# Performance work log

Measured on AMD Instinct MI355X. Metric: run time of the kernel, lower is better.

Reference implementation:

```python
import jax, jax.numpy as jnp
import numpy as np

B, N, K = 64, 1024, 16  # graphs per batch, nodes per graph, top-k (k=16 hardcoded in module)
EPS = 1e-20


def setup_inputs() -> dict:
    key = jax.random.key(0)
    ks = jax.random.split(key, 6)
    C = 128
    x = jax.random.normal(ks[0], (B * N, C), jnp.float32)
    pos = jax.random.normal(ks[1], (B * N, 3), jnp.float32)
    W1 = jax.random.normal(ks[2], (C, C), jnp.float32) / np.sqrt(C).astype(np.float32)
    b1 = jnp.zeros((C,), jnp.float32)
    gamma = jnp.ones((C,), jnp.float32)
    beta = jnp.zeros((C,), jnp.float32)
    W2 = jax.random.normal(ks[3], (C, 10), jnp.float32) / np.sqrt(C).astype(np.float32)
    b2 = jnp.zeros((10,), jnp.float32)
    t = jnp.ones((1,), jnp.float32)
    return dict(x=x, pos=pos, W1=W1, b1=b1, gamma=gamma, beta=beta, W2=W2, b2=b2, t=t)


def _edge_arrays(idx):
    # idx: (B, N, K) per-target top-k source node indices (graph-local)
    offs = (jnp.arange(B, dtype=jnp.int32) * N)[:, None, None]
    src = (idx + offs).reshape(-1)
    tgt = (jnp.broadcast_to(jnp.arange(N, dtype=jnp.int32)[None, :, None], (B, N, K)) + offs).reshape(-1)
    return jnp.stack([src, tgt])  # (2, B*N*K)


def _knn_edges(pos):
    # KNNGraph(k=16) on positions, loop=False (exclude self)
    p = pos.reshape(B, N, 3)
    d2 = jnp.sum((p[:, :, None, :] - p[:, None, :, :]) ** 2, axis=-1)  # (B,N,N)
    d2 = d2 + jnp.eye(N, dtype=d2.dtype) * 1e10
    _, idx = jax.lax.top_k(-d2, K)  # nearest K per node
    return _edge_arrays(idx)


def reference(x, pos, W1, b1, gamma, beta, W2, b2, t):
    key = jax.random.key(42)
    k1, k2 = jax.random.split(key)
    # tg MLP: lin -> batchnorm -> relu -> lin (training-mode batch stats over nodes)
    h = x @ W1 + b1
    mu = h.mean(axis=0)
    var = h.var(axis=0)
    h = (h - mu) / jnp.sqrt(var + 1e-5) * gamma + beta
    h = jax.nn.relu(h)
    emb = h @ W2 + b2  # (B*N, 10)
    emb = emb + jax.random.uniform(k1, emb.shape, emb.dtype) * 0.001
    e = emb.reshape(B, N, 10)
    # pairwise distances per graph (vectorized over the python loop in the original)
    diff = e[:, :, None, :] - e[:, None, :, :]  # (B,N,N,10)
    dist = jnp.linalg.norm(diff, axis=-1)  # (B,N,N)
    p = jnp.exp(-t[0] * dist ** 2)
    u = jax.random.uniform(k2, p.shape, p.dtype)
    gumbel = -jnp.log(-jnp.log(u + EPS) + EPS)
    noisy_logits = jnp.log(p + EPS) + gumbel
    # torch topk over dim=0 (sources) for each target column -> transpose then top_k on last axis
    vals, idx = jax.lax.top_k(jnp.swapaxes(noisy_logits, 1, 2), K)  # (B,N,K)
    vals = jax.nn.softmax(vals, axis=-1)
    vals = vals / vals.max(axis=-1, keepdims=True)
    soft_idx = _edge_arrays(idx)  # (2, B*N*K)
    knn_idx = _knn_edges(pos)
    edge_index = jnp.concatenate([soft_idx, knn_idx], axis=1)
    return vals.reshape(-1), soft_idx, edge_index
```

## Files before the change

kernel.cpp:

```cpp
#include <hip/hip_runtime.h>
#include <stdint.h>
#include <math.h>

#define BG 64
#define NG 1024
#define KK 16
#define CC 128
#define NNODE (BG * NG)
#define NSOFT (BG * NG * KK)
#define FEPS 1e-20f

__host__ __device__ __forceinline__ uint32_t rotl32u(uint32_t x, int r) {
  return (x << r) | (x >> (32 - r));
}

__host__ __device__ __forceinline__ void tf2x32(uint32_t k0, uint32_t k1,
                                                uint32_t x0, uint32_t x1,
                                                uint32_t &o0, uint32_t &o1) {
  uint32_t k2 = k0 ^ k1 ^ 0x1BD11BDAu;
  x0 += k0; x1 += k1;
#define TFR(r) { x0 += x1; x1 = rotl32u(x1, r); x1 ^= x0; }
  TFR(13) TFR(15) TFR(26) TFR(6)
  x0 += k1; x1 += k2 + 1u;
  TFR(17) TFR(29) TFR(16) TFR(24)
  x0 += k2; x1 += k0 + 2u;
  TFR(13) TFR(15) TFR(26) TFR(6)
  x0 += k0; x1 += k1 + 3u;
  TFR(17) TFR(29) TFR(16) TFR(24)
  x0 += k1; x1 += k2 + 4u;
  TFR(13) TFR(15) TFR(26) TFR(6)
  x0 += k2; x1 += k0 + 5u;
#undef TFR
  o0 = x0; o1 = x1;
}

__device__ __forceinline__ float jax_uniform01(uint32_t ka, uint32_t kb, uint32_t m) {
  uint32_t o0, o1;
  tf2x32(ka, kb, 0u, m, o0, o1);
  uint32_t bits = o0 ^ o1;
  float f = __uint_as_float((bits >> 9) | 0x3f800000u) - 1.0f;
  return fmaxf(f, 0.0f);
}

__device__ __forceinline__ int vbin_soft(float v) {
  float fb = (v + 50.0f) * (256.0f / 67.0f);
  fb = fminf(fmaxf(fb, 0.0f), 255.0f);
  return (int)fb;
}
__device__ __forceinline__ int vbin_knn(float v) {
  float fb = (v + 64.0f) * 4.0f;
  fb = fminf(fmaxf(fb, 0.0f), 255.0f);
  return (int)fb;
}

#define LDS_WAIT() asm volatile("s_waitcnt lgkmcnt(0)" ::: "memory")

__global__ __launch_bounds__(256) void k_gemm1(const float* __restrict__ x,
                                               const float* __restrict__ W1,
                                               const float* __restrict__ b1,
                                               float* __restrict__ h) {
  __shared__ __align__(16) float xs[64 * 128];
  const int t = threadIdx.x;
  const size_t blockBase = (size_t)blockIdx.x * (64 * 128);
  #pragma unroll
  for (int j = 0; j < 32; ++j) xs[t + j * 256] = x[blockBase + t + j * 256];
  __syncthreads();
  const int c = t & 127;
  const int rg = t >> 7;
  float acc[32];
  #pragma unroll
  for (int j = 0; j < 32; ++j) acc[j] = 0.f;
  const float* xrow = &xs[rg * 32 * 128];
  for (int k4 = 0; k4 < 128; k4 += 4) {
    const float w0 = W1[(size_t)(k4 + 0) * 128 + c];
    const float w1 = W1[(size_t)(k4 + 1) * 128 + c];
    const float w2 = W1[(size_t)(k4 + 2) * 128 + c];
    const float w3 = W1[(size_t)(k4 + 3) * 128 + c];
    #pragma unroll
    for (int j = 0; j < 32; ++j) {
      const float4 xv = *(const float4*)&xrow[j * 128 + k4];
      acc[j] = fmaf(xv.x, w0, acc[j]);
      acc[j] = fmaf(xv.y, w1, acc[j]);
      acc[j] = fmaf(xv.z, w2, acc[j]);
      acc[j] = fmaf(xv.w, w3, acc[j]);
    }
  }
  const float bb = b1[c];
  #pragma unroll
  for (int j = 0; j < 32; ++j)
    h[blockBase + (size_t)(rg * 32 + j) * 128 + c] = acc[j] + bb;
}

__global__ __launch_bounds__(256) void k_bn_part(const float* __restrict__ h,
                                                 float* __restrict__ p1,
                                                 float* __restrict__ p2) {
  const int t = threadIdx.x;
  const int cg = t & 31;
  const int rg = t >> 5;
  const size_t rowBase = (size_t)blockIdx.x * 256;
  float s1[4] = {0, 0, 0, 0}, s2[4] = {0, 0, 0, 0};
  for (int i = 0; i < 32; ++i) {
    const size_t r = rowBase + (size_t)i * 8 + rg;
    const float4 v = *(const float4*)&h[r * 128 + cg * 4];
    s1[0] += v.x; s2[0] = fmaf(v.x, v.x, s2[0]);
    s1[1] += v.y; s2[1] = fmaf(v.y, v.y, s2[1]);
    s1[2] += v.z; s2[2] = fmaf(v.z, v.z, s2[2]);
    s1[3] += v.w; s2[3] = fmaf(v.w, v.w, s2[3]);
  }
  __shared__ float red1[8 * 128];
  __shared__ float red2[8 * 128];
  #pragma unroll
  for (int i = 0; i < 4; ++i) {
    red1[rg * 128 + cg * 4 + i] = s1[i];
    red2[rg * 128 + cg * 4 + i] = s2[i];
  }
  __syncthreads();
  if (t < 128) {
    float a = 0.f;
    #pragma unroll
    for (int g = 0; g < 8; ++g) a += red1[g * 128 + t];
    p1[(size_t)blockIdx.x * 128 + t] = a;
  } else {
    const int c = t - 128;
    float a = 0.f;
    #pragma unroll
    for (int g = 0; g < 8; ++g) a += red2[g * 128 + c];
    p2[(size_t)blockIdx.x * 128 + c] = a;
  }
}

__global__ __launch_bounds__(128) void k_bn_final(const float* __restrict__ p1,
                                                  const float* __restrict__ p2,
                                                  const float* __restrict__ gamma,
                                                  const float* __restrict__ beta,
                                                  float* __restrict__ scale,
                                                  float* __restrict__ shift) {
  const int c = threadIdx.x;
  float s1 = 0.f, s2 = 0.f;
  for (int b = 0; b < 256; ++b) {
    s1 += p1[b * 128 + c];
    s2 += p2[b * 128 + c];
  }
  const float mu = s1 * (1.0f / NNODE);
  float var = s2 * (1.0f / NNODE) - mu * mu;
  var = fmaxf(var, 0.f);
  const float sc = gamma[c] / sqrtf(var + 1e-5f);
  scale[c] = sc;
  shift[c] = beta[c] - mu * sc;
}

__global__ __launch_bounds__(256) void k_emb(const float* __restrict__ h,
                                             const float* __restrict__ scale,
                                             const float* __restrict__ shift,
                                             const float* __restrict__ W2,
                                             const float* __restrict__ b2,
                                             float* __restrict__ e,
                                             uint32_t ka, uint32_t kb) {
  __shared__ __align__(16) float hn[64 * 132];
  const int t = threadIdx.x;
  const int rowBase = blockIdx.x * 64;
  {
    const int c = t & 127;
    const float sc = scale[c], sh = shift[c];
    #pragma unroll
    for (int j = 0; j < 32; ++j) {
      const int r = (t >> 7) + j * 2;
      const float v = fmaf(h[(size_t)(rowBase + r) * 128 + c], sc, sh);
      hn[r * 132 + c] = fmaxf(v, 0.f);
    }
  }
  __syncthreads();
  #pragma unroll
  for (int j = 0; j < 3; ++j) {
    const int o = t + j * 256;
    if (o < 640) {
      const int r = o / 10;
      const int col = o - r * 10;
      float acc = 0.f;
      for (int k4 = 0; k4 < 128; k4 += 4) {
        const float4 hv = *(const float4*)&hn[r * 132 + k4];
        acc = fmaf(hv.x, W2[(k4 + 0) * 10 + col], acc);
        acc = fmaf(hv.y, W2[(k4 + 1) * 10 + col], acc);
        acc = fmaf(hv.z, W2[(k4 + 2) * 10 + col], acc);
        acc = fmaf(hv.w, W2[(k4 + 3) * 10 + col], acc);
      }
      acc += b2[col];
      const uint32_t m = (uint32_t)(rowBase + r) * 10u + (uint32_t)col;
      const float u = jax_uniform01(ka, kb, m);
      e[(size_t)(rowBase + r) * 10 + col] = acc + u * 0.001f;
    }
  }
}

__global__ __launch_bounds__(512) void k_soft(const float* __restrict__ e,
                                              const float* __restrict__ tsc,
                                              float* __restrict__ out,
                                              uint32_t ka, uint32_t kb) {
  __shared__ uint32_t bins[8][256];
  __shared__ float    cv[8][64];
  __shared__ int      cidx[8][64];
  __shared__ uint32_t cnt[8];
  __shared__ float    o16v[8][16];
  __shared__ int      o16i[8][16];

  const int t = threadIdx.x, lane = t & 63, w = t >> 6;
  const int node = blockIdx.x * 8 + w;
  const int b = node >> 10, jt = node & (NG - 1);
  const float negt = -tsc[0];
  const float* eg = e + (size_t)b * (NG * 10);

  { uint4 z = {0, 0, 0, 0}; *(uint4*)&bins[w][lane * 4] = z; }
  if (lane == 0) cnt[w] = 0u;
  LDS_WAIT();

  float ej[10];
  #pragma unroll
  for (int d = 0; d < 10; ++d) ej[d] = eg[(size_t)jt * 10 + d];

  float vv[16];
  const uint32_t mB = ((uint32_t)b << 20) + (uint32_t)jt;
  #pragma unroll
  for (int st = 0; st < 16; ++st) {
    const int s = st * 64 + lane;
    const float2* rp = (const float2*)(eg + (size_t)s * 10);
    const float2 a0 = rp[0], a1 = rp[1], a2 = rp[2], a3 = rp[3], a4 = rp[4];
    float dd, acc;
    dd = ej[0] - a0.x; acc = dd * dd;
    dd = ej[1] - a0.y; acc = fmaf(dd, dd, acc);
    dd = ej[2] - a1.x; acc = fmaf(dd, dd, acc);
    dd = ej[3] - a1.y; acc = fmaf(dd, dd, acc);
    dd = ej[4] - a2.x; acc = fmaf(dd, dd, acc);
    dd = ej[5] - a2.y; acc = fmaf(dd, dd, acc);
    dd = ej[6] - a3.x; acc = fmaf(dd, dd, acc);
    dd = ej[7] - a3.y; acc = fmaf(dd, dd, acc);
    dd = ej[8] - a4.x; acc = fmaf(dd, dd, acc);
    dd = ej[9] - a4.y; acc = fmaf(dd, dd, acc);
    const float dist = sqrtf(acc);
    const float d2 = dist * dist;
    const float p = __expf(negt * d2);
    const float u = jax_uniform01(ka, kb, mB + ((uint32_t)s << 10));
    const float li = __logf(u + FEPS);
    const float g = -__logf(FEPS - li);
    const float v = __logf(p + FEPS) + g;
    vv[st] = v;
    atomicAdd(&bins[w][vbin_soft(v)], 1u);
  }
  LDS_WAIT();

  const uint4 c4 = *(const uint4*)&bins[w][lane * 4];
  const uint32_t lsum = c4.x + c4.y + c4.z + c4.w;
  uint32_t xs = lsum;
  #pragma unroll
  for (int off = 1; off < 64; off <<= 1) {
    uint32_t tt = (uint32_t)__shfl_down((int)xs, off, 64);
    if (lane + off < 64) xs += tt;
  }
  const uint32_t after = xs - lsum;
  const uint32_t s3 = c4.w + after;
  const uint32_t s2 = c4.z + s3;
  const uint32_t s1 = c4.y + s2;
  const uint32_t s0 = c4.x + s1;
  int localB = -1;
  if (s3 >= 16u) localB = lane * 4 + 3;
  else if (s2 >= 16u) localB = lane * 4 + 2;
  else if (s1 >= 16u) localB = lane * 4 + 1;
  else if (s0 >= 16u) localB = lane * 4 + 0;
  const unsigned long long msk = __ballot(localB >= 0);
  const int hl = 63 - __builtin_clzll(msk);
  const int B = __shfl(localB, hl, 64);

  #pragma unroll
  for (int st = 0; st < 16; ++st) {
    if (vbin_soft(vv[st]) >= B) {
      const uint32_t pos = atomicAdd(&cnt[w], 1u);
      if (pos < 64u) { cv[w][pos] = vv[st]; cidx[w][pos] = st * 64 + lane; }
    }
  }
  LDS_WAIT();

  int C = (int)cnt[w]; if (C > 64) C = 64;
  const float mvv = (lane < C) ? cv[w][lane] : 0.f;
  const int   mii = (lane < C) ? cidx[w][lane] : 0;
  int rank = 0;
  for (int j = 0; j < C; ++j) {
    const float vj = cv[w][j];
    const int ij = cidx[w][j];
    if (vj > mvv || (vj == mvv && ij < mii)) ++rank;
  }
  if (lane < C && rank < 16) { o16v[w][rank] = mvv; o16i[w][rank] = mii; }
  LDS_WAIT();

  if (lane < 16) {
    const float vq = o16v[w][lane];
    const float m0 = o16v[w][0];
    float uex = __expf(vq - m0);
    float ss = uex;
    #pragma unroll
    for (int off = 1; off < 16; off <<= 1) ss += __shfl_xor(ss, off, 16);
    const float u0 = __shfl(uex, 0, 16);
    const float s0v = u0 / ss;
    const float sv = uex / ss;
    const float o = sv / s0v;
    const size_t base = (size_t)node * KK + lane;
    const float tgtf = (float)node;
    const float srcf = (float)(b * NG + o16i[w][lane]);
    out[base] = o;
    out[(size_t)NSOFT + base] = srcf;
    out[2 * (size_t)NSOFT + base] = tgtf;
    out[3 * (size_t)NSOFT + base] = srcf;
    out[5 * (size_t)NSOFT + base] = tgtf;
  }
}

__global__ __launch_bounds__(512) void k_knn(const float* __restrict__ pos,
                                             float* __restrict__ out) {
  __shared__ uint32_t bins[8][256];
  __shared__ float    cv[8][64];
  __shared__ int      cidx[8][64];
  __shared__ uint32_t cnt[8];
  __shared__ int      o16i[8][16];

  const int t = threadIdx.x, lane = t & 63, w = t >> 6;
  const int node = blockIdx.x * 8 + w;
  const int b = node >> 10, it = node & (NG - 1);
  const float* pg = pos + (size_t)b * (NG * 3);

  { uint4 z = {0, 0, 0, 0}; *(uint4*)&bins[w][lane * 4] = z; }
  if (lane == 0) cnt[w] = 0u;
  LDS_WAIT();

  const float px = pg[(size_t)it * 3 + 0];
  const float py = pg[(size_t)it * 3 + 1];
  const float pz = pg[(size_t)it * 3 + 2];

  float vv[16];
  #pragma unroll
  for (int st = 0; st < 16; ++st) {
    const int s = st * 64 + lane;
    const float qx = pg[(size_t)s * 3 + 0];
    const float qy = pg[(size_t)s * 3 + 1];
    const float qz = pg[(size_t)s * 3 + 2];
    const float dx = px - qx, dy = py - qy, dz = pz - qz;
    float d2 = dx * dx;
    d2 = fmaf(dy, dy, d2);
    d2 = fmaf(dz, dz, d2);
    if (s == it) d2 += 1e10f;
    const float v = -d2;
    vv[st] = v;
    atomicAdd(&bins[w][vbin_knn(v)], 1u);
  }
  LDS_WAIT();

  const uint4 c4 = *(const uint4*)&bins[w][lane * 4];
  const uint32_t lsum = c4.x + c4.y + c4.z + c4.w;
  uint32_t xs = lsum;
  #pragma unroll
  for (int off = 1; off < 64; off <<= 1) {
    uint32_t tt = (uint32_t)__shfl_down((int)xs, off, 64);
    if (lane + off < 64) xs += tt;
  }
  const uint32_t after = xs - lsum;
  const uint32_t s3 = c4.w + after;
  const uint32_t s2 = c4.z + s3;
  const uint32_t s1 = c4.y + s2;
  const uint32_t s0 = c4.x + s1;
  int localB = -1;
  if (s3 >= 16u) localB = lane * 4 + 3;
  else if (s2 >= 16u) localB = lane * 4 + 2;
  else if (s1 >= 16u) localB = lane * 4 + 1;
  else if (s0 >= 16u) localB = lane * 4 + 0;
  const unsigned long long msk = __ballot(localB >= 0);
  const int hl = 63 - __builtin_clzll(msk);
  const int B = __shfl(localB, hl, 64);

  #pragma unroll
  for (int st = 0; st < 16; ++st) {
    if (vbin_knn(vv[st]) >= B) {
      const uint32_t pos = atomicAdd(&cnt[w], 1u);
      if (pos < 64u) { cv[w][pos] = vv[st]; cidx[w][pos] = st * 64 + lane; }
    }
  }
  LDS_WAIT();

  int C = (int)cnt[w]; if (C > 64) C = 64;
  const float mvv = (lane < C) ? cv[w][lane] : 0.f;
  const int   mii = (lane < C) ? cidx[w][lane] : 0;
  int rank = 0;
  for (int j = 0; j < C; ++j) {
    const float vj = cv[w][j];
    const int ij = cidx[w][j];
    if (vj > mvv || (vj == mvv && ij < mii)) ++rank;
  }
  if (lane < C && rank < 16) o16i[w][rank] = mii;
  LDS_WAIT();

  if (lane < 16) {
    const size_t base = (size_t)node * KK + lane;
    out[4 * (size_t)NSOFT + base] = (float)(b * NG + o16i[w][lane]);
    out[6 * (size_t)NSOFT + base] = (float)node;
  }
}

extern "C" void kernel_launch(void* const* d_in, const int* in_sizes, int n_in,
                              void* d_out, int out_size, void* d_ws, size_t ws_size,
                              hipStream_t stream) {
  const float* x     = (const float*)d_in[0];
  const float* pos   = (const float*)d_in[1];
  const float* W1    = (const float*)d_in[2];
  const float* b1    = (const float*)d_in[3];
  const float* gamma = (const float*)d_in[4];
  const float* beta  = (const float*)d_in[5];
  const float* W2    = (const float*)d_in[6];
  const float* b2    = (const float*)d_in[7];
  const float* t     = (const float*)d_in[8];
  float* out = (float*)d_out;

  float* ws    = (float*)d_ws;
  float* h     = ws;
  float* e     = h + (size_t)NNODE * CC;
  float* p1    = e + (size_t)NNODE * 10;
  float* p2    = p1 + 256 * 128;
  float* scale = p2 + 256 * 128;
  float* shift = scale + CC;

  uint32_t k1a, k1b, k2a, k2b;
  tf2x32(0u, 42u, 0u, 0u, k1a, k1b);
  tf2x32(0u, 42u, 0u, 1u, k2a, k2b);

  k_gemm1<<<dim3(NNODE / 64), dim3(256), 0, stream>>>(x, W1, b1, h);
  k_bn_part<<<dim3(256), dim3(256), 0, stream>>>(h, p1, p2);
  k_bn_final<<<dim3(1), dim3(128), 0, stream>>>(p1, p2, gamma, beta, scale, shift);
  k_emb<<<dim3(NNODE / 64), dim3(256), 0, stream>>>(h, scale, shift, W2, b2, e, k1a, k1b);
  k_knn<<<dim3(NNODE / 8), dim3(512), 0, stream>>>(pos, out);
  k_soft<<<dim3(NNODE / 8), dim3(512), 0, stream>>>(e, t, out, k2a, k2b);
}
```

Measured before the change: 447.7 us.

## Fuse BN partial stats into GEMM, parallelize BN final, stage graph data in LDS

Measured after the change: 419.8 us. -6.2%, faster.

```diff
diff --git a/kernel.cpp b/kernel.cpp
--- a/kernel.cpp
+++ b/kernel.cpp
@@ -58,7 +58,9 @@
 __global__ __launch_bounds__(256) void k_gemm1(const float* __restrict__ x,
                                                const float* __restrict__ W1,
                                                const float* __restrict__ b1,
-                                               float* __restrict__ h) {
+                                               float* __restrict__ h,
+                                               float* __restrict__ p1,
+                                               float* __restrict__ p2) {
   __shared__ __align__(16) float xs[64 * 128];
   const int t = threadIdx.x;
   const size_t blockBase = (size_t)blockIdx.x * (64 * 128);
@@ -86,67 +88,54 @@
     }
   }
   const float bb = b1[c];
-  #pragma unroll
-  for (int j = 0; j < 32; ++j)
-    h[blockBase + (size_t)(rg * 32 + j) * 128 + c] = acc[j] + bb;
-}
-
-__global__ __launch_bounds__(256) void k_bn_part(const float* __restrict__ h,
-                                                 float* __restrict__ p1,
-                                                 float* __restrict__ p2) {
-  const int t = threadIdx.x;
-  const int cg = t & 31;
-  const int rg = t >> 5;
-  const size_t rowBase = (size_t)blockIdx.x * 256;
-  float s1[4] = {0, 0, 0, 0}, s2[4] = {0, 0, 0, 0};
-  for (int i = 0; i < 32; ++i) {
-    const size_t r = rowBase + (size_t)i * 8 + rg;
-    const float4 v = *(const float4*)&h[r * 128 + cg * 4];
-    s1[0] += v.x; s2[0] = fmaf(v.x, v.x, s2[0]);
-    s1[1] += v.y; s2[1] = fmaf(v.y, v.y, s2[1]);
-    s1[2] += v.z; s2[2] = fmaf(v.z, v.z, s2[2]);
-    s1[3] += v.w; s2[3] = fmaf(v.w, v.w, s2[3]);
-  }
-  __shared__ float red1[8 * 128];
-  __shared__ float red2[8 * 128];
-  #pragma unroll
-  for (int i = 0; i < 4; ++i) {
-    red1[rg * 128 + cg * 4 + i] = s1[i];
-    red2[rg * 128 + cg * 4 + i] = s2[i];
-  }
+  float s1 = 0.f, s2 = 0.f;
+  #pragma unroll
+  for (int j = 0; j < 32; ++j) {
+    const float v = acc[j] + bb;
+    h[blockBase + (size_t)(rg * 32 + j) * 128 + c] = v;
+    s1 += v;
+    s2 = fmaf(v, v, s2);
+  }
+  __syncthreads();
+  float* r1 = xs;
+  float* r2 = xs + 256;
+  r1[rg * 128 + c] = s1;
+  r2[rg * 128 + c] = s2;
   __syncthreads();
   if (t < 128) {
-    float a = 0.f;
-    #pragma unroll
-    for (int g = 0; g < 8; ++g) a += red1[g * 128 + t];
-    p1[(size_t)blockIdx.x * 128 + t] = a;
+    p1[(size_t)t * 1024 + blockIdx.x] = r1[t] + r1[128 + t];
   } else {
-    const int c = t - 128;
-    float a = 0.f;
-    #pragma unroll
-    for (int g = 0; g < 8; ++g) a += red2[g * 128 + c];
-    p2[(size_t)blockIdx.x * 128 + c] = a;
-  }
-}
-
-__global__ __launch_bounds__(128) void k_bn_final(const float* __restrict__ p1,
+    const int cc = t - 128;
+    p2[(size_t)cc * 1024 + blockIdx.x] = r2[cc] + r2[128 + cc];
+  }
+}
+
+__global__ __launch_bounds__(256) void k_bn_final(const float* __restrict__ p1,
                                                   const float* __restrict__ p2,
                                                   const float* __restrict__ gamma,
                                                   const float* __restrict__ beta,
                                                   float* __restrict__ scale,
                                                   float* __restrict__ shift) {
-  const int c = threadIdx.x;
-  float s1 = 0.f, s2 = 0.f;
-  for (int b = 0; b < 256; ++b) {
-    s1 += p1[b * 128 + c];
-    s2 += p2[b * 128 + c];
-  }
-  const float mu = s1 * (1.0f / NNODE);
-  float var = s2 * (1.0f / NNODE) - mu * mu;
-  var = fmaxf(var, 0.f);
-  const float sc = gamma[c] / sqrtf(var + 1e-5f);
-  scale[c] = sc;
-  shift[c] = beta[c] - mu * sc;
+  const int c = blockIdx.x, t = threadIdx.x;
+  const float* q1 = p1 + (size_t)c * 1024;
+  const float* q2 = p2 + (size_t)c * 1024;
+  float a1 = q1[t] + q1[t + 256] + q1[t + 512] + q1[t + 768];
+  float a2 = q2[t] + q2[t + 256] + q2[t + 512] + q2[t + 768];
+  __shared__ float r1[256], r2[256];
+  r1[t] = a1; r2[t] = a2;
+  __syncthreads();
+  for (int o = 128; o > 0; o >>= 1) {
+    if (t < o) { r1[t] += r1[t + o]; r2[t] += r2[t + o]; }
+    __syncthreads();
+  }
+  if (t == 0) {
+    const float mu = r1[0] * (1.0f / NNODE);
+    float var = r2[0] * (1.0f / NNODE) - mu * mu;
+    var = fmaxf(var, 0.f);
+    const float sc = gamma[c] / sqrtf(var + 1e-5f);
+    scale[c] = sc;
+    shift[c] = beta[c] - mu * sc;
+  }
 }
 
 __global__ __launch_bounds__(256) void k_emb(const float* __restrict__ h,
@@ -196,49 +185,59 @@
                                               const float* __restrict__ tsc,
                                               float* __restrict__ out,
                                               uint32_t ka, uint32_t kb) {
+  __shared__ float    els[10 * NG];
   __shared__ uint32_t bins[8][256];
-  __shared__ float    cv[8][64];
-  __shared__ int      cidx[8][64];
+  __shared__ float    cv[8][48];
+  __shared__ int      cidx[8][48];
   __shared__ uint32_t cnt[8];
   __shared__ float    o16v[8][16];
   __shared__ int      o16i[8][16];
 
   const int t = threadIdx.x, lane = t & 63, w = t >> 6;
   const int node = blockIdx.x * 8 + w;
-  const int b = node >> 10, jt = node & (NG - 1);
+  const int b = blockIdx.x >> 7;
+  const int jt = node & (NG - 1);
   const float negt = -tsc[0];
   const float* eg = e + (size_t)b * (NG * 10);
 
   { uint4 z = {0, 0, 0, 0}; *(uint4*)&bins[w][lane * 4] = z; }
   if (lane == 0) cnt[w] = 0u;
-  LDS_WAIT();
+
+  for (int s = t; s < NG; s += 512) {
+    const float2* rp = (const float2*)(eg + (size_t)s * 10);
+    const float2 a0 = rp[0], a1 = rp[1], a2 = rp[2], a3 = rp[3], a4 = rp[4];
+    els[0 * NG + s] = a0.x; els[1 * NG + s] = a0.y;
+    els[2 * NG + s] = a1.x; els[3 * NG + s] = a1.y;
+    els[4 * NG + s] = a2.x; els[5 * NG + s] = a2.y;
+    els[6 * NG + s] = a3.x; els[7 * NG + s] = a3.y;
+    els[8 * NG + s] = a4.x; els[9 * NG + s] = a4.y;
+  }
+  __syncthreads();
 
   float ej[10];
   #pragma unroll
-  for (int d = 0; d < 10; ++d) ej[d] = eg[(size_t)jt * 10 + d];
+  for (int d = 0; d < 10; ++d) ej[d] = els[d * NG + jt];
 
   float vv[16];
-  const uint32_t mB = ((uint32_t)b << 20) + (uint32_t)jt;
+  const uint32_t mL = ((uint32_t)b << 20) + (uint32_t)jt + ((uint32_t)lane << 10);
   #pragma unroll
   for (int st = 0; st < 16; ++st) {
     const int s = st * 64 + lane;
-    const float2* rp = (const float2*)(eg + (size_t)s * 10);
-    const float2 a0 = rp[0], a1 = rp[1], a2 = rp[2], a3 = rp[3], a4 = rp[4];
     float dd, acc;
-    dd = ej[0] - a0.x; acc = dd * dd;
-    dd = ej[1] - a0.y; acc = fmaf(dd, dd, acc);
-    dd = ej[2] - a1.x; acc = fmaf(dd, dd, acc);
-    dd = ej[3] - a1.y; acc = fmaf(dd, dd, acc);
-    dd = ej[4] - a2.x; acc = fmaf(dd, dd, acc);
-    dd = ej[5] - a2.y; acc = fmaf(dd, dd, acc);
-    dd = ej[6] - a3.x; acc = fmaf(dd, dd, acc);
-    dd = ej[7] - a3.y; acc = fmaf(dd, dd, acc);
-    dd = ej[8] - a4.x; acc = fmaf(dd, dd, acc);
-    dd = ej[9] - a4.y; acc = fmaf(dd, dd, acc);
+    dd = ej[0] - els[0 * NG + s]; acc = dd * dd;
+    dd = ej[1] - els[1 * NG + s]; acc = fmaf(dd, dd, acc);
+    dd = ej[2] - els[2 * NG + s]; acc = fmaf(dd, dd, acc);
+    dd = ej[3] - els[3 * NG + s]; acc = fmaf(dd, dd, acc);
+    dd = ej[4] - els[4 * NG + s]; acc = fmaf(dd, dd, acc);
+    dd = ej[5] - els[5 * NG + s]; acc = fmaf(dd, dd, acc);
+    dd = ej[6] - els[6 * NG + s]; acc = fmaf(dd, dd, acc);
+    dd = ej[7] - els[7 * NG + s]; acc = fmaf(dd, dd, acc);
+    dd = ej[8] - els[8 * NG + s]; acc = fmaf(dd, dd, acc);
+    dd = ej[9] - els[9 * NG + s]; acc = fmaf(dd, dd, acc);
     const float dist = sqrtf(acc);
     const float d2 = dist * dist;
     const float p = __expf(negt * d2);
-    const float u = jax_uniform01(ka, kb, mB + ((uint32_t)s << 10));
+    const float u = jax_uniform01(ka, kb, mL + ((uint32_t)st << 16));
     const float li = __logf(u + FEPS);
     const float g = -__logf(FEPS - li);
     const float v = __logf(p + FEPS) + g;
@@ -273,12 +272,12 @@
   for (int st = 0; st < 16; ++st) {
     if (vbin_soft(vv[st]) >= B) {
       const uint32_t pos = atomicAdd(&cnt[w], 1u);
-      if (pos < 64u) { cv[w][pos] = vv[st]; cidx[w][pos] = st * 64 + lane; }
+      if (pos < 48u) { cv[w][pos] = vv[st]; cidx[w][pos] = st * 64 + lane; }
     }
   }
   LDS_WAIT();
 
-  int C = (int)cnt[w]; if (C > 64) C = 64;
+  int C = (int)cnt[w]; if (C > 48) C = 48;
   const float mvv = (lane < C) ? cv[w][lane] : 0.f;
   const int   mii = (lane < C) ? cidx[w][lane] : 0;
   int rank = 0;
@@ -314,33 +313,40 @@
 
 __global__ __launch_bounds__(512) void k_knn(const float* __restrict__ pos,
                                              float* __restrict__ out) {
+  __shared__ float    pls[3 * NG];
   __shared__ uint32_t bins[8][256];
-  __shared__ float    cv[8][64];
-  __shared__ int      cidx[8][64];
+  __shared__ float    cv[8][48];
+  __shared__ int      cidx[8][48];
   __shared__ uint32_t cnt[8];
   __shared__ int      o16i[8][16];
 
   const int t = threadIdx.x, lane = t & 63, w = t >> 6;
   const int node = blockIdx.x * 8 + w;
-  const int b = node >> 10, it = node & (NG - 1);
+  const int b = blockIdx.x >> 7;
+  const int it = node & (NG - 1);
   const float* pg = pos + (size_t)b * (NG * 3);
 
   { uint4 z = {0, 0, 0, 0}; *(uint4*)&bins[w][lane * 4] = z; }
   if (lane == 0) cnt[w] = 0u;
-  LDS_WAIT();
-
-  const float px = pg[(size_t)it * 3 + 0];
-  const float py = pg[(size_t)it * 3 + 1];
-  const float pz = pg[(size_t)it * 3 + 2];
+
+  for (int s = t; s < NG; s += 512) {
+    pls[0 * NG + s] = pg[(size_t)s * 3 + 0];
+    pls[1 * NG + s] = pg[(size_t)s * 3 + 1];
+    pls[2 * NG + s] = pg[(size_t)s * 3 + 2];
+  }
+  __syncthreads();
+
+  const float px = pls[0 * NG + it];
+  const float py = pls[1 * NG + it];
+  const float pz = pls[2 * NG + it];
 
   float vv[16];
   #pragma unroll
   for (int st = 0; st < 16; ++st) {
     const int s = st * 64 + lane;
-    const float qx = pg[(size_t)s * 3 + 0];
-    const float qy = pg[(size_t)s * 3 + 1];
-    const float qz = pg[(size_t)s * 3 + 2];
-    const float dx = px - qx, dy = py - qy, dz = pz - qz;
+    const float dx = px - pls[0 * NG + s];
+    const float dy = py - pls[1 * NG + s];
+    const float dz = pz - pls[2 * NG + s];
     float d2 = dx * dx;
     d2 = fmaf(dy, dy, d2);
     d2 = fmaf(dz, dz, d2);
@@ -377,12 +383,12 @@
   for (int st = 0; st < 16; ++st) {
     if (vbin_knn(vv[st]) >= B) {
       const uint32_t pos = atomicAdd(&cnt[w], 1u);
-      if (pos < 64u) { cv[w][pos] = vv[st]; cidx[w][pos] = st * 64 + lane; }
+      if (pos < 48u) { cv[w][pos] = vv[st]; cidx[w][pos] = st * 64 + lane; }
     }
   }
   LDS_WAIT();
 
-  int C = (int)cnt[w]; if (C > 64) C = 64;
+  int C = (int)cnt[w]; if (C > 48) C = 48;
   const float mvv = (lane < C) ? cv[w][lane] : 0.f;
   const int   mii = (lane < C) ? cidx[w][lane] : 0;
   int rank = 0;
@@ -419,17 +425,16 @@
   float* h     = ws;
   float* e     = h + (size_t)NNODE * CC;
   float* p1    = e + (size_t)NNODE * 10;
-  float* p2    = p1 + 256 * 128;
-  float* scale = p2 + 256 * 128;
+  float* p2    = p1 + 128 * 1024;
+  float* scale = p2 + 128 * 1024;
   float* shift = scale + CC;
 
   uint32_t k1a, k1b, k2a, k2b;
   tf2x32(0u, 42u, 0u, 0u, k1a, k1b);
   tf2x32(0u, 42u, 0u, 1u, k2a, k2b);
 
-  k_gemm1<<<dim3(NNODE / 64), dim3(256), 0, stream>>>(x, W1, b1, h);
-  k_bn_part<<<dim3(256), dim3(256), 0, stream>>>(h, p1, p2);
-  k_bn_final<<<dim3(1), dim3(128), 0, stream>>>(p1, p2, gamma, beta, scale, shift);
+  k_gemm1<<<dim3(NNODE / 64), dim3(256), 0, stream>>>(x, W1, b1, h, p1, p2);
+  k_bn_final<<<dim3(CC), dim3(256), 0, stream>>>(p1, p2, gamma, beta, scale, shift);
   k_emb<<<dim3(NNODE / 64), dim3(256), 0, stream>>>(h, scale, shift, W2, b2, e, k1a, k1b);
   k_knn<<<dim3(NNODE / 8), dim3(512), 0, stream>>>(pos, out);
   k_soft<<<dim3(NNODE / 8), dim3(512), 0, stream>>>(e, t, out, k2a, k2b);
```
